# Performance work log

Hardware: AMD Instinct MI355X
Metric: run time of the kernel (lower is better)

The kernel has to match this reference:

```python
import jax, jax.numpy as jnp
import numpy as np

EPS = 1e-05
BITW = 8
BITA = 8


def _ste_round(v):
    # round with identity gradient (TF Round->Identity override)
    return v + jax.lax.stop_gradient(jnp.round(v) - v)


def _quantize_overflow(x, bits):
    # tensorlayer _quantize_overflow: linear quantization over [min, max]
    n = 2.0 ** bits - 1.0
    mx = jnp.max(x)
    mn = jnp.min(x)
    step = jax.lax.stop_gradient((mx - mn) / n)
    return _ste_round((x - mn) / step) * step + mn


def _conv2d_same(x, w):
    # x: [N,H,W,C], w: [KH,KW,C,F]
    return jax.lax.conv_general_dilated(
        x, w, window_strides=(1, 1), padding='SAME',
        dimension_numbers=('NHWC', 'HWIO', 'NHWC'))


def setup_inputs() -> dict:
    key = jax.random.key(0)
    k1, k2 = jax.random.split(key)
    x = jax.random.normal(k1, (32, 56, 56, 128), dtype=jnp.float32)
    W = jax.random.normal(k2, (3, 3, 128, 256), dtype=jnp.float32) * 0.02
    gamma = jnp.ones((256,), dtype=jnp.float32)
    beta = jnp.zeros((256,), dtype=jnp.float32)
    return {"x": x, "W": W, "gamma": gamma, "beta": beta}


def reference(x, W, gamma, beta):
    # 1) fake-quantize activations
    xq = _quantize_overflow(x, BITA)
    # 2) full-precision conv to get batch statistics (training path)
    conv_out = _conv2d_same(x, W)  # [N,H,W,F]
    mean = jnp.mean(conv_out, axis=(0, 1, 2))          # [F]
    var = jnp.var(conv_out, axis=(0, 1, 2))            # [F], biased (tf.nn.moments)
    inv_std = 1.0 / jnp.sqrt(var + EPS)                # [F]
    # 3) fold BN into weights/bias
    w_fold = W * (gamma * inv_std)                     # broadcast over [KH,KW,C,F]
    bias_fold = beta - gamma * mean * inv_std          # [F]
    # 4) quantize folded weights, conv with quantized activations
    wq = _quantize_overflow(w_fold, BITW)
    out = _conv2d_same(xq, wq) + bias_fold
    return jax.nn.relu(out)
```

## Files before the change

### kernel.cpp

```cpp
#include <hip/hip_runtime.h>

typedef float f32x4_t __attribute__((ext_vector_type(4)));
typedef __bf16 bf16x8_t __attribute__((ext_vector_type(8)));
typedef unsigned short u16x8_t __attribute__((ext_vector_type(8)));

#define NPIX        100352
#define PIX_PER_IMG 3136
#define PH          58
#define PPIX        3364
#define C_IN        128
#define C_OUT       256
#define NV4         3211264
#define NWELEM      294912
#define MTILES      392
#define NPADPIX     107648

#define OFF_ENC     0
#define OFF_SCALE   64
#define OFF_BIAS    1152
#define OFF_WT      4096
#define OFF_WQT     593920
#define OFF_PSUM    1183744
#define OFF_WFMIN   1585152
#define OFF_WFMAX   1586176
#define OFF_PSQ     1986560
#define OFF_XPAD    2789376
#define OFF_XQPAD   30347264

__device__ __forceinline__ unsigned short f2bf(float x) {
  unsigned u = __float_as_uint(x);
  u += 0x7FFFu + ((u >> 16) & 1u);
  return (unsigned short)(u >> 16);
}
__device__ __forceinline__ unsigned encf(float v) {
  unsigned u = __float_as_uint(v);
  return (u & 0x80000000u) ? ~u : (u | 0x80000000u);
}
__device__ __forceinline__ float decf(unsigned e) {
  unsigned u = (e & 0x80000000u) ? (e ^ 0x80000000u) : ~e;
  return __uint_as_float(u);
}
__device__ __forceinline__ void gl_lds16(const void* g, void* l) {
  auto gp = (const __attribute__((address_space(1))) unsigned*)(const unsigned*)g;
  auto lp = (__attribute__((address_space(3))) unsigned*)(unsigned*)l;
  __builtin_amdgcn_global_load_lds(gp, lp, 16, 0, 0);
}
#define SCHED_FENCE() __builtin_amdgcn_sched_barrier(0)

__global__ void kinit(unsigned* enc) {
  enc[0] = 0xFFFFFFFFu; enc[1] = 0u;
  enc[2] = 0xFFFFFFFFu; enc[3] = 0u;
}

__global__ void kminmax(const float4* __restrict__ x, unsigned* __restrict__ enc) {
  const int tid = blockIdx.x * blockDim.x + threadIdx.x;
  const int stride = gridDim.x * blockDim.x;
  float mn = 3.4e38f, mx = -3.4e38f;
  for (int i = tid; i < NV4; i += stride) {
    float4 v = x[i];
    mn = fminf(mn, fminf(fminf(v.x, v.y), fminf(v.z, v.w)));
    mx = fmaxf(mx, fmaxf(fmaxf(v.x, v.y), fmaxf(v.z, v.w)));
  }
  #pragma unroll
  for (int off = 32; off > 0; off >>= 1) {
    mn = fminf(mn, __shfl_xor(mn, off));
    mx = fmaxf(mx, __shfl_xor(mx, off));
  }
  __shared__ float smn[4], smx[4];
  const int lane = threadIdx.x & 63, w = threadIdx.x >> 6;
  if (lane == 0) { smn[w] = mn; smx[w] = mx; }
  __syncthreads();
  if (threadIdx.x == 0) {
    mn = fminf(fminf(smn[0], smn[1]), fminf(smn[2], smn[3]));
    mx = fmaxf(fmaxf(smx[0], smx[1]), fmaxf(smx[2], smx[3]));
    atomicMin(&enc[0], encf(mn));
    atomicMax(&enc[1], encf(mx));
  }
}

__global__ void kwq(const float* __restrict__ W, const float* __restrict__ scale,
                    const unsigned* __restrict__ enc, unsigned short* __restrict__ wqt) {
  const int idx = blockIdx.x * 256 + threadIdx.x;
  if (idx >= NWELEM) return;
  const int c = idx & 127;
  const int f = (idx >> 7) & 255;
  const int tap = idx >> 15;
  const float wmn = decf(enc[2]), wmx = decf(enc[3]);
  const float wstep = (wmx - wmn) / 255.0f;
  const float wrstep = 255.0f / (wmx - wmn);
  const float v = W[(tap * 128 + c) * 256 + f] * scale[f];
  const float q = rintf((v - wmn) * wrstep) * wstep + wmn;
  wqt[idx] = f2bf(q);
}

__global__ void kpadfill(const float* __restrict__ x, const unsigned* __restrict__ enc,
                         unsigned short* __restrict__ xpad, unsigned short* __restrict__ xqpad,
                         const float* __restrict__ W, unsigned short* __restrict__ wtt,
                         float* __restrict__ wfmin, float* __restrict__ wfmax)
{
  if (blockIdx.x >= 7880) {
    const int f = blockIdx.x - 7880;
    float mn = 3.4e38f, mx = -3.4e38f;
    for (int e = threadIdx.x; e < 1152; e += 256) {
      const float v = W[e * 256 + f];
      mn = fminf(mn, v); mx = fmaxf(mx, v);
    }
    #pragma unroll
    for (int off = 32; off > 0; off >>= 1) {
      mn = fminf(mn, __shfl_xor(mn, off));
      mx = fmaxf(mx, __shfl_xor(mx, off));
    }
    __shared__ float rmn[4], rmx[4];
    const int lane = threadIdx.x & 63, w = threadIdx.x >> 6;
    if (lane == 0) { rmn[w] = mn; rmx[w] = mx; }
    __syncthreads();
    if (threadIdx.x == 0) {
      wfmin[f] = fminf(fminf(rmn[0], rmn[1]), fminf(rmn[2], rmn[3]));
      wfmax[f] = fmaxf(fmaxf(rmx[0], rmx[1]), fmaxf(rmx[2], rmx[3]));
    }
    return;
  }
  if (blockIdx.x >= 6728) {
    const int idx = (blockIdx.x - 6728) * 256 + threadIdx.x;
    if (idx < NWELEM) {
      const int c = idx & 127;
      const int f = (idx >> 7) & 255;
      const int tap = idx >> 15;
      wtt[idx] = f2bf(W[(tap * 128 + c) * 256 + f]);
    }
    return;
  }
  const int tid = blockIdx.x * 256 + threadIdx.x;
  if (tid >= NPADPIX * 16) return;
  const int pp = tid >> 4;
  const int c8 = (tid & 15) << 3;
  const int n = pp / PPIX;
  const int rem = pp - n * PPIX;
  const int hp = rem / PH;
  const int wp = rem - hp * PH;
  u16x8_t vb, vq;
  #pragma unroll
  for (int j = 0; j < 8; ++j) { vb[j] = 0; vq[j] = 0; }
  if (hp >= 1 && hp <= 56 && wp >= 1 && wp <= 56) {
    const float mn = decf(enc[0]), mx = decf(enc[1]);
    const float step = (mx - mn) / 255.0f, rstep = 255.0f / (mx - mn);
    const float* src = x + ((n * PIX_PER_IMG) + (hp - 1) * 56 + (wp - 1)) * C_IN + c8;
    const float4 a = *(const float4*)src;
    const float4 b = *(const float4*)(src + 4);
    const float v[8] = {a.x, a.y, a.z, a.w, b.x, b.y, b.z, b.w};
    #pragma unroll
    for (int j = 0; j < 8; ++j) {
      vb[j] = f2bf(v[j]);
      const float qv = rintf((v[j] - mn) * rstep) * step + mn;
      vq[j] = f2bf(qv);
    }
  }
  *(u16x8_t*)(xpad + pp * C_IN + c8) = vb;
  *(u16x8_t*)(xqpad + pp * C_IN + c8) = vq;
}

template<int STATS>
__global__ __launch_bounds__(512, 4)
void kconv(const unsigned short* __restrict__ xin,
           const unsigned short* __restrict__ wt,
           float* __restrict__ out,
           const float* __restrict__ bias,
           float* __restrict__ psum,
           float* __restrict__ psq)
{
  const int bid = blockIdx.x;
  const int slot = (bid & 7) * 98 + (bid >> 3);
  const int bm = slot >> 1;
  const int bn = slot & 1;

  const int tid = threadIdx.x;
  const int lane = tid & 63;
  const int wid = tid >> 6;
  const int wm = wid >> 1;
  const int wn = wid & 1;
  const int l16 = lane & 15;
  const int rsub = lane >> 4;

  __shared__ __align__(16) unsigned char smem[49152];

  unsigned aoff[2];
  {
    const int arow0 = wid * 8 + (lane >> 3);
    const int pc = lane & 7;
    #pragma unroll
    for (int j = 0; j < 2; ++j) {
      const int row = j * 64 + arow0;
      const int lc = pc ^ (row & 7);
      const int pix = bm * 256 + row + 128 * (lc >> 2);
      const int n = pix / PIX_PER_IMG;
      const int rem = pix - n * PIX_PER_IMG;
      const int hh = rem / 56;
      const int ww = rem - hh * 56;
      aoff[j] = (unsigned)((n * PPIX + hh * PH + ww) * C_IN + (lc & 3) * 8);
    }
  }
  unsigned boff;
  {
    const int row = wid * 8 + (lane >> 3);
    const int pc = lane & 7;
    const int lc = pc ^ (row & 7);
    const int f = bn * 128 + row + 64 * (lc >> 2);
    boff = (unsigned)(f * C_IN + (lc & 3) * 8);
  }

  int a_rd[4], b_rd[4];
  #pragma unroll
  for (int im = 0; im < 4; ++im) {
    const int p = wm * 64 + im * 16 + l16;
    const int row = p & 127, half = p >> 7;
    const int phys = (half * 4 + rsub) ^ (row & 7);
    a_rd[im] = row * 128 + phys * 16;
  }
  #pragma unroll
  for (int in = 0; in < 4; ++in) {
    const int f = wn * 64 + in * 16 + l16;
    const int row = f & 63, half = f >> 6;
    const int phys = (half * 4 + rsub) ^ (row & 7);
    b_rd[in] = row * 128 + phys * 16;
  }

  f32x4_t acc[4][4];
  #pragma unroll
  for (int im = 0; im < 4; ++im)
    #pragma unroll
    for (int in = 0; in < 4; ++in)
      #pragma unroll
      for (int j = 0; j < 4; ++j) acc[im][in][j] = 0.f;

  auto stage = [&](int s) {
    const int tap = s >> 2;
    const int cq = (s & 3) * 32;
    const int kh = tap / 3, kw = tap - kh * 3;
    const unsigned atap = (unsigned)((kh * PH + kw) * C_IN + cq);
    const unsigned btap = (unsigned)(tap * (C_OUT * C_IN) + cq);
    unsigned char* sA = smem + (s & 1) * 24576;
    unsigned char* sB = sA + 16384;
    gl_lds16(xin + atap + aoff[0], sA + wid * 1024);
    gl_lds16(xin + atap + aoff[1], sA + 8192 + wid * 1024);
    gl_lds16(wt + btap + boff, sB + wid * 1024);
  };

  auto compute = [&](int s) {
    const unsigned char* sA = smem + (s & 1) * 24576;
    const unsigned char* sB = sA + 16384;
    bf16x8_t av[4], bv[4];
    #pragma unroll
    for (int im = 0; im < 4; ++im) av[im] = *(const bf16x8_t*)(sA + a_rd[im]);
    #pragma unroll
    for (int in = 0; in < 4; ++in) bv[in] = *(const bf16x8_t*)(sB + b_rd[in]);
    #pragma unroll
    for (int im = 0; im < 4; ++im)
      #pragma unroll
      for (int in = 0; in < 4; ++in)
        acc[im][in] = __builtin_amdgcn_mfma_f32_16x16x32_bf16(av[im], bv[in], acc[im][in], 0, 0, 0);
  };

  stage(0);
  stage(1);

  #pragma unroll 1
  for (int s = 0; s < 35; ++s) {
    asm volatile("s_waitcnt vmcnt(3)" ::: "memory");
    SCHED_FENCE();
    __builtin_amdgcn_s_barrier();
    SCHED_FENCE();
    compute(s);
    SCHED_FENCE();
    __builtin_amdgcn_s_barrier();
    SCHED_FENCE();
    if (s < 34) stage(s + 2);
  }
  asm volatile("s_waitcnt vmcnt(0)" ::: "memory");
  SCHED_FENCE();
  __builtin_amdgcn_s_barrier();
  SCHED_FENCE();
  compute(35);

  if (STATS) {
    __syncthreads();
    float* sb = (float*)smem;
    #pragma unroll
    for (int in = 0; in < 4; ++in) {
      float s = 0.f, q = 0.f;
      #pragma unroll
      for (int im = 0; im < 4; ++im)
        #pragma unroll
        for (int j = 0; j < 4; ++j) {
          const float v = acc[im][in][j];
          s += v; q += v * v;
        }
      s += __shfl_xor(s, 16); q += __shfl_xor(q, 16);
      s += __shfl_xor(s, 32); q += __shfl_xor(q, 32);
      if (lane < 16) {
        sb[wid * 64 + in * 16 + lane] = s;
        sb[512 + wid * 64 + in * 16 + lane] = q;
      }
    }
    __syncthreads();
    if (tid < 128) {
      const int wn2 = tid >> 6, cl = tid & 63;
      float s = 0.f, q = 0.f;
      #pragma unroll
      for (int wm2 = 0; wm2 < 4; ++wm2) {
        s += sb[(wm2 * 2 + wn2) * 64 + cl];
        q += sb[512 + (wm2 * 2 + wn2) * 64 + cl];
      }
      psum[(bm * 2 + bn) * 128 + tid] = s;
      psq[(bm * 2 + bn) * 128 + tid] = q;
    }
  } else {
    float bval[4];
    #pragma unroll
    for (int in = 0; in < 4; ++in)
      bval[in] = bias[bn * 128 + wn * 64 + in * 16 + l16];
    #pragma unroll
    for (int im = 0; im < 4; ++im) {
      #pragma unroll
      for (int j = 0; j < 4; ++j) {
        const int pix = bm * 256 + wm * 64 + im * 16 + rsub * 4 + j;
        #pragma unroll
        for (int in = 0; in < 4; ++in) {
          const int f = bn * 128 + wn * 64 + in * 16 + l16;
          out[pix * 256 + f] = fmaxf(acc[im][in][j] + bval[in], 0.f);
        }
      }
    }
  }
}

__global__ __launch_bounds__(256)
void kstats(const float* __restrict__ psum, const float* __restrict__ psq,
            const float* __restrict__ gamma, const float* __restrict__ beta,
            float* __restrict__ scale, float* __restrict__ bias,
            const float* __restrict__ wfmin, const float* __restrict__ wfmax,
            unsigned* __restrict__ enc)
{
  const int ch = blockIdx.x;
  const int bn = ch >> 7, col = ch & 127;
  float s = 0.f, q = 0.f;
  for (int bm = threadIdx.x; bm < MTILES; bm += 256) {
    s += psum[(bm * 2 + bn) * 128 + col];
    q += psq[(bm * 2 + bn) * 128 + col];
  }
  #pragma unroll
  for (int off = 32; off > 0; off >>= 1) {
    s += __shfl_xor(s, off);
    q += __shfl_xor(q, off);
  }
  __shared__ float ss[4], sq2[4];
  const int lane = threadIdx.x & 63, w = threadIdx.x >> 6;
  if (lane == 0) { ss[w] = s; sq2[w] = q; }
  __syncthreads();
  if (threadIdx.x == 0) {
    s = ss[0] + ss[1] + ss[2] + ss[3];
    q = sq2[0] + sq2[1] + sq2[2] + sq2[3];
    const float inv = 1.0f / (float)NPIX;
    const float mean = s * inv;
    const float var = q * inv - mean * mean;
    const float istd = 1.0f / sqrtf(var + 1e-5f);
    const float g = gamma[ch];
    const float sc = g * istd;
    scale[ch] = sc;
    bias[ch] = beta[ch] - g * mean * istd;
    const float p0 = sc * wfmin[ch];
    const float p1 = sc * wfmax[ch];
    atomicMin(&enc[2], encf(fminf(p0, p1)));
    atomicMax(&enc[3], encf(fmaxf(p0, p1)));
  }
}

extern "C" void kernel_launch(void* const* d_in, const int* in_sizes, int n_in,
                              void* d_out, int out_size, void* d_ws, size_t ws_size,
                              hipStream_t stream)
{
  const float* x     = (const float*)d_in[0];
  const float* W     = (const float*)d_in[1];
  const float* gamma = (const float*)d_in[2];
  const float* beta  = (const float*)d_in[3];
  float* out = (float*)d_out;
  char* ws = (char*)d_ws;

  unsigned* enc        = (unsigned*)(ws + OFF_ENC);
  float* scale         = (float*)(ws + OFF_SCALE);
  float* bias          = (float*)(ws + OFF_BIAS);
  unsigned short* Wt   = (unsigned short*)(ws + OFF_WT);
  unsigned short* Wqt  = (unsigned short*)(ws + OFF_WQT);
  float* psum          = (float*)(ws + OFF_PSUM);
  float* wfmin         = (float*)(ws + OFF_WFMIN);
  float* wfmax         = (float*)(ws + OFF_WFMAX);
  float* psq           = (float*)(ws + OFF_PSQ);
  unsigned short* xpad  = (unsigned short*)(ws + OFF_XPAD);
  unsigned short* xqpad = (unsigned short*)(ws + OFF_XQPAD);

  kinit<<<1, 64, 0, stream>>>(enc);
  kminmax<<<1024, 256, 0, stream>>>((const float4*)x, enc);
  kpadfill<<<8136, 256, 0, stream>>>(x, enc, xpad, xqpad, W, Wt, wfmin, wfmax);
  kconv<1><<<784, 512, 0, stream>>>(xpad, Wt, nullptr, nullptr, psum, psq);
  kstats<<<256, 256, 0, stream>>>(psum, psq, gamma, beta, scale, bias, wfmin, wfmax, enc);
  kwq<<<1152, 256, 0, stream>>>(W, scale, enc, Wqt);
  kconv<0><<<784, 512, 0, stream>>>(xqpad, Wqt, out, bias, nullptr, nullptr);
}
```

Before: 215.5 us.

## Shrink conv tiles to 128x128 and load weights directly into registers

The implicit-GEMM conv kernel moves from 512-thread 256x128 tiles to 256-thread 128x128 tiles, which doubles the grid to 1568 blocks and cuts LDS use to 16KB. The weight (B) operand no longer goes through shared memory. Each wave loads it straight from global memory into registers with inline global_load_dwordx4, double-buffered across two unrolled pipeline stages. This is meant to raise occupancy and drop LDS traffic for B, but each wave now fetches weights separately, so there is less reuse and more global and L2 load traffic. The partial-stats buffers and the stats reduction grow to match the doubled number of M tiles.

```diff
diff --git a/kernel.cpp b/kernel.cpp
--- a/kernel.cpp
+++ b/kernel.cpp
@@ -12,7 +12,7 @@
 #define C_OUT       256
 #define NV4         3211264
 #define NWELEM      294912
-#define MTILES      392
+#define MT128       784
 #define NPADPIX     107648
 
 #define OFF_ENC     0
@@ -21,11 +21,11 @@
 #define OFF_WT      4096
 #define OFF_WQT     593920
 #define OFF_PSUM    1183744
-#define OFF_WFMIN   1585152
-#define OFF_WFMAX   1586176
-#define OFF_PSQ     1986560
-#define OFF_XPAD    2789376
-#define OFF_XQPAD   30347264
+#define OFF_WFMIN   1988608
+#define OFF_WFMAX   1989632
+#define OFF_PSQ     1990656
+#define OFF_XPAD    2793472
+#define OFF_XQPAD   30351360
 
 __device__ __forceinline__ unsigned short f2bf(float x) {
   unsigned u = __float_as_uint(x);
@@ -160,7 +160,7 @@
 }
 
 template<int STATS>
-__global__ __launch_bounds__(512, 4)
+__global__ __launch_bounds__(256, 3)
 void kconv(const unsigned short* __restrict__ xin,
            const unsigned short* __restrict__ wt,
            float* __restrict__ out,
@@ -169,7 +169,7 @@
            float* __restrict__ psq)
 {
   const int bid = blockIdx.x;
-  const int slot = (bid & 7) * 98 + (bid >> 3);
+  const int slot = (bid & 7) * 196 + (bid >> 3);
   const int bm = slot >> 1;
   const int bn = slot & 1;
 
@@ -181,17 +181,16 @@
   const int l16 = lane & 15;
   const int rsub = lane >> 4;
 
-  __shared__ __align__(16) unsigned char smem[49152];
+  __shared__ __align__(16) unsigned char smem[16384];
 
   unsigned aoff[2];
   {
-    const int arow0 = wid * 8 + (lane >> 3);
-    const int pc = lane & 7;
+    const int pc = tid & 7;
     #pragma unroll
     for (int j = 0; j < 2; ++j) {
-      const int row = j * 64 + arow0;
+      const int row = j * 32 + (tid >> 3);
       const int lc = pc ^ (row & 7);
-      const int pix = bm * 256 + row + 128 * (lc >> 2);
+      const int pix = bm * 128 + row + 64 * (lc >> 2);
       const int n = pix / PIX_PER_IMG;
       const int rem = pix - n * PIX_PER_IMG;
       const int hh = rem / 56;
@@ -199,29 +198,19 @@
       aoff[j] = (unsigned)((n * PPIX + hh * PH + ww) * C_IN + (lc & 3) * 8);
     }
   }
-  unsigned boff;
-  {
-    const int row = wid * 8 + (lane >> 3);
-    const int pc = lane & 7;
-    const int lc = pc ^ (row & 7);
-    const int f = bn * 128 + row + 64 * (lc >> 2);
-    boff = (unsigned)(f * C_IN + (lc & 3) * 8);
-  }
-
-  int a_rd[4], b_rd[4];
+  int a_rd[4];
   #pragma unroll
   for (int im = 0; im < 4; ++im) {
     const int p = wm * 64 + im * 16 + l16;
-    const int row = p & 127, half = p >> 7;
+    const int row = p & 63, half = p >> 6;
     const int phys = (half * 4 + rsub) ^ (row & 7);
     a_rd[im] = row * 128 + phys * 16;
   }
+  unsigned boffB[4];
   #pragma unroll
   for (int in = 0; in < 4; ++in) {
-    const int f = wn * 64 + in * 16 + l16;
-    const int row = f & 63, half = f >> 6;
-    const int phys = (half * 4 + rsub) ^ (row & 7);
-    b_rd[in] = row * 128 + phys * 16;
+    const int f = bn * 128 + wn * 64 + in * 16 + l16;
+    boffB[in] = (unsigned)(f * C_IN + rsub * 8) * 2u;
   }
 
   f32x4_t acc[4][4];
@@ -237,22 +226,28 @@
     const int cq = (s & 3) * 32;
     const int kh = tap / 3, kw = tap - kh * 3;
     const unsigned atap = (unsigned)((kh * PH + kw) * C_IN + cq);
-    const unsigned btap = (unsigned)(tap * (C_OUT * C_IN) + cq);
-    unsigned char* sA = smem + (s & 1) * 24576;
-    unsigned char* sB = sA + 16384;
+    unsigned char* sA = smem + (s & 1) * 8192;
     gl_lds16(xin + atap + aoff[0], sA + wid * 1024);
-    gl_lds16(xin + atap + aoff[1], sA + 8192 + wid * 1024);
-    gl_lds16(wt + btap + boff, sB + wid * 1024);
+    gl_lds16(xin + atap + aoff[1], sA + 4096 + wid * 1024);
   };
 
-  auto compute = [&](int s) {
-    const unsigned char* sA = smem + (s & 1) * 24576;
-    const unsigned char* sB = sA + 16384;
-    bf16x8_t av[4], bv[4];
+  auto loadB = [&](int s, bf16x8_t (&bv)[4]) {
+    const int tap = s >> 2;
+    const int cq = (s & 3) * 32;
+    const unsigned short* base = wt + tap * (C_OUT * C_IN) + cq;
+    #pragma unroll
+    for (int in = 0; in < 4; ++in)
+      asm volatile("global_load_dwordx4 %0, %1, %2"
+                   : "=v"(bv[in])
+                   : "v"(boffB[in]), "s"(base)
+                   : "memory");
+  };
+
+  auto compute = [&](int s, bf16x8_t (&bv)[4]) {
+    const unsigned char* sA = smem + (s & 1) * 8192;
+    bf16x8_t av[4];
     #pragma unroll
     for (int im = 0; im < 4; ++im) av[im] = *(const bf16x8_t*)(sA + a_rd[im]);
-    #pragma unroll
-    for (int in = 0; in < 4; ++in) bv[in] = *(const bf16x8_t*)(sB + b_rd[in]);
     #pragma unroll
     for (int im = 0; im < 4; ++im)
       #pragma unroll
@@ -260,26 +255,32 @@
         acc[im][in] = __builtin_amdgcn_mfma_f32_16x16x32_bf16(av[im], bv[in], acc[im][in], 0, 0, 0);
   };
 
-  stage(0);
-  stage(1);
+  bf16x8_t bvA[4], bvB[4];
+  stage(0); loadB(0, bvA);
+  stage(1); loadB(1, bvB);
 
   #pragma unroll 1
-  for (int s = 0; s < 35; ++s) {
-    asm volatile("s_waitcnt vmcnt(3)" ::: "memory");
+  for (int s = 0; s < 36; s += 2) {
+    asm volatile("s_waitcnt vmcnt(6)" ::: "memory");
     SCHED_FENCE();
     __builtin_amdgcn_s_barrier();
     SCHED_FENCE();
-    compute(s);
+    compute(s, bvA);
     SCHED_FENCE();
     __builtin_amdgcn_s_barrier();
     SCHED_FENCE();
-    if (s < 34) stage(s + 2);
-  }
-  asm volatile("s_waitcnt vmcnt(0)" ::: "memory");
-  SCHED_FENCE();
-  __builtin_amdgcn_s_barrier();
-  SCHED_FENCE();
-  compute(35);
+    if (s + 2 < 36) { stage(s + 2); loadB(s + 2, bvA); }
+    if (s + 1 < 35) asm volatile("s_waitcnt vmcnt(6)" ::: "memory");
+    else            asm volatile("s_waitcnt vmcnt(0)" ::: "memory");
+    SCHED_FENCE();
+    __builtin_amdgcn_s_barrier();
+    SCHED_FENCE();
+    compute(s + 1, bvB);
+    SCHED_FENCE();
+    __builtin_amdgcn_s_barrier();
+    SCHED_FENCE();
+    if (s + 3 < 36) { stage(s + 3); loadB(s + 3, bvB); }
+  }
 
   if (STATS) {
     __syncthreads();
@@ -298,18 +299,14 @@
       s += __shfl_xor(s, 32); q += __shfl_xor(q, 32);
       if (lane < 16) {
         sb[wid * 64 + in * 16 + lane] = s;
-        sb[512 + wid * 64 + in * 16 + lane] = q;
+        sb[256 + wid * 64 + in * 16 + lane] = q;
       }
     }
     __syncthreads();
     if (tid < 128) {
       const int wn2 = tid >> 6, cl = tid & 63;
-      float s = 0.f, q = 0.f;
-      #pragma unroll
-      for (int wm2 = 0; wm2 < 4; ++wm2) {
-        s += sb[(wm2 * 2 + wn2) * 64 + cl];
-        q += sb[512 + (wm2 * 2 + wn2) * 64 + cl];
-      }
+      const float s = sb[wn2 * 64 + cl] + sb[(2 + wn2) * 64 + cl];
+      const float q = sb[256 + wn2 * 64 + cl] + sb[256 + (2 + wn2) * 64 + cl];
       psum[(bm * 2 + bn) * 128 + tid] = s;
       psq[(bm * 2 + bn) * 128 + tid] = q;
     }
@@ -322,7 +319,7 @@
     for (int im = 0; im < 4; ++im) {
       #pragma unroll
       for (int j = 0; j < 4; ++j) {
-        const int pix = bm * 256 + wm * 64 + im * 16 + rsub * 4 + j;
+        const int pix = bm * 128 + wm * 64 + im * 16 + rsub * 4 + j;
         #pragma unroll
         for (int in = 0; in < 4; ++in) {
           const int f = bn * 128 + wn * 64 + in * 16 + l16;
@@ -343,7 +340,7 @@
   const int ch = blockIdx.x;
   const int bn = ch >> 7, col = ch & 127;
   float s = 0.f, q = 0.f;
-  for (int bm = threadIdx.x; bm < MTILES; bm += 256) {
+  for (int bm = threadIdx.x; bm < MT128; bm += 256) {
     s += psum[(bm * 2 + bn) * 128 + col];
     q += psq[(bm * 2 + bn) * 128 + col];
   }
@@ -400,8 +397,8 @@
   kinit<<<1, 64, 0, stream>>>(enc);
   kminmax<<<1024, 256, 0, stream>>>((const float4*)x, enc);
   kpadfill<<<8136, 256, 0, stream>>>(x, enc, xpad, xqpad, W, Wt, wfmin, wfmax);
-  kconv<1><<<784, 512, 0, stream>>>(xpad, Wt, nullptr, nullptr, psum, psq);
+  kconv<1><<<1568, 256, 0, stream>>>(xpad, Wt, nullptr, nullptr, psum, psq);
   kstats<<<256, 256, 0, stream>>>(psum, psq, gamma, beta, scale, bias, wfmin, wfmax, enc);
   kwq<<<1152, 256, 0, stream>>>(W, scale, enc, Wqt);
-  kconv<0><<<784, 512, 0, stream>>>(xqpad, Wqt, out, bias, nullptr, nullptr);
-}
+  kconv<0><<<1568, 256, 0, stream>>>(xqpad, Wqt, out, bias, nullptr, nullptr);
+}
```

Result: slower. 333.6 us (+54.8%).

## Fuse min/max into padding pass and overlap quantized-input fill with stats conv

Applied to the files above, without the earlier changes.

Computes the activation min/max inside the bf16 padding kernel, so the separate min/max pass over x goes away. The quantized padded-input fill and the per-channel weight min/max move into extra blocks of the stats convolution launch, where they can overlap the GEMM blocks. The init kernel becomes a memset, and max is stored as min of the inverted encoding so that a single 0xFF fill initialises both slots. The cost is a larger, heterogeneous conv grid and a second read of x inside the conv launch.

```diff
diff --git a/kernel.cpp b/kernel.cpp
--- a/kernel.cpp
+++ b/kernel.cpp
@@ -10,7 +10,6 @@
 #define PPIX        3364
 #define C_IN        128
 #define C_OUT       256
-#define NV4         3211264
 #define NWELEM      294912
 #define MTILES      392
 #define NPADPIX     107648
@@ -47,20 +46,45 @@
 }
 #define SCHED_FENCE() __builtin_amdgcn_sched_barrier(0)
 
-__global__ void kinit(unsigned* enc) {
-  enc[0] = 0xFFFFFFFFu; enc[1] = 0u;
-  enc[2] = 0xFFFFFFFFu; enc[3] = 0u;
-}
-
-__global__ void kminmax(const float4* __restrict__ x, unsigned* __restrict__ enc) {
-  const int tid = blockIdx.x * blockDim.x + threadIdx.x;
-  const int stride = gridDim.x * blockDim.x;
+__global__ __launch_bounds__(256)
+void kprep1(const float* __restrict__ x, unsigned short* __restrict__ xpad,
+            const float* __restrict__ W, unsigned short* __restrict__ wtt,
+            unsigned* __restrict__ enc)
+{
+  if (blockIdx.x >= 6728) {
+    const int idx = (blockIdx.x - 6728) * 256 + threadIdx.x;
+    if (idx < NWELEM) {
+      const int c = idx & 127;
+      const int f = (idx >> 7) & 255;
+      const int tap = idx >> 15;
+      wtt[idx] = f2bf(W[(tap * 128 + c) * 256 + f]);
+    }
+    return;
+  }
+  const int tid = blockIdx.x * 256 + threadIdx.x;
+  const int pp = tid >> 4;
+  const int c8 = (tid & 15) << 3;
+  const int n = pp / PPIX;
+  const int rem = pp - n * PPIX;
+  const int hp = rem / PH;
+  const int wp = rem - hp * PH;
+  u16x8_t vb;
+  #pragma unroll
+  for (int j = 0; j < 8; ++j) vb[j] = 0;
   float mn = 3.4e38f, mx = -3.4e38f;
-  for (int i = tid; i < NV4; i += stride) {
-    float4 v = x[i];
-    mn = fminf(mn, fminf(fminf(v.x, v.y), fminf(v.z, v.w)));
-    mx = fmaxf(mx, fmaxf(fmaxf(v.x, v.y), fmaxf(v.z, v.w)));
-  }
+  if (hp >= 1 && hp <= 56 && wp >= 1 && wp <= 56) {
+    const float* src = x + ((n * PIX_PER_IMG) + (hp - 1) * 56 + (wp - 1)) * C_IN + c8;
+    const float4 a = *(const float4*)src;
+    const float4 b = *(const float4*)(src + 4);
+    const float v[8] = {a.x, a.y, a.z, a.w, b.x, b.y, b.z, b.w};
+    #pragma unroll
+    for (int j = 0; j < 8; ++j) {
+      vb[j] = f2bf(v[j]);
+      mn = fminf(mn, v[j]);
+      mx = fmaxf(mx, v[j]);
+    }
+  }
+  *(u16x8_t*)(xpad + pp * C_IN + c8) = vb;
   #pragma unroll
   for (int off = 32; off > 0; off >>= 1) {
     mn = fminf(mn, __shfl_xor(mn, off));
@@ -74,7 +98,7 @@
     mn = fminf(fminf(smn[0], smn[1]), fminf(smn[2], smn[3]));
     mx = fmaxf(fmaxf(smx[0], smx[1]), fmaxf(smx[2], smx[3]));
     atomicMin(&enc[0], encf(mn));
-    atomicMax(&enc[1], encf(mx));
+    atomicMin(&enc[1], ~encf(mx));
   }
 }
 
@@ -85,78 +109,12 @@
   const int c = idx & 127;
   const int f = (idx >> 7) & 255;
   const int tap = idx >> 15;
-  const float wmn = decf(enc[2]), wmx = decf(enc[3]);
+  const float wmn = decf(enc[2]), wmx = decf(~enc[3]);
   const float wstep = (wmx - wmn) / 255.0f;
   const float wrstep = 255.0f / (wmx - wmn);
   const float v = W[(tap * 128 + c) * 256 + f] * scale[f];
   const float q = rintf((v - wmn) * wrstep) * wstep + wmn;
   wqt[idx] = f2bf(q);
-}
-
-__global__ void kpadfill(const float* __restrict__ x, const unsigned* __restrict__ enc,
-                         unsigned short* __restrict__ xpad, unsigned short* __restrict__ xqpad,
-                         const float* __restrict__ W, unsigned short* __restrict__ wtt,
-                         float* __restrict__ wfmin, float* __restrict__ wfmax)
-{
-  if (blockIdx.x >= 7880) {
-    const int f = blockIdx.x - 7880;
-    float mn = 3.4e38f, mx = -3.4e38f;
-    for (int e = threadIdx.x; e < 1152; e += 256) {
-      const float v = W[e * 256 + f];
-      mn = fminf(mn, v); mx = fmaxf(mx, v);
-    }
-    #pragma unroll
-    for (int off = 32; off > 0; off >>= 1) {
-      mn = fminf(mn, __shfl_xor(mn, off));
-      mx = fmaxf(mx, __shfl_xor(mx, off));
-    }
-    __shared__ float rmn[4], rmx[4];
-    const int lane = threadIdx.x & 63, w = threadIdx.x >> 6;
-    if (lane == 0) { rmn[w] = mn; rmx[w] = mx; }
-    __syncthreads();
-    if (threadIdx.x == 0) {
-      wfmin[f] = fminf(fminf(rmn[0], rmn[1]), fminf(rmn[2], rmn[3]));
-      wfmax[f] = fmaxf(fmaxf(rmx[0], rmx[1]), fmaxf(rmx[2], rmx[3]));
-    }
-    return;
-  }
-  if (blockIdx.x >= 6728) {
-    const int idx = (blockIdx.x - 6728) * 256 + threadIdx.x;
-    if (idx < NWELEM) {
-      const int c = idx & 127;
-      const int f = (idx >> 7) & 255;
-      const int tap = idx >> 15;
-      wtt[idx] = f2bf(W[(tap * 128 + c) * 256 + f]);
-    }
-    return;
-  }
-  const int tid = blockIdx.x * 256 + threadIdx.x;
-  if (tid >= NPADPIX * 16) return;
-  const int pp = tid >> 4;
-  const int c8 = (tid & 15) << 3;
-  const int n = pp / PPIX;
-  const int rem = pp - n * PPIX;
-  const int hp = rem / PH;
-  const int wp = rem - hp * PH;
-  u16x8_t vb, vq;
-  #pragma unroll
-  for (int j = 0; j < 8; ++j) { vb[j] = 0; vq[j] = 0; }
-  if (hp >= 1 && hp <= 56 && wp >= 1 && wp <= 56) {
-    const float mn = decf(enc[0]), mx = decf(enc[1]);
-    const float step = (mx - mn) / 255.0f, rstep = 255.0f / (mx - mn);
-    const float* src = x + ((n * PIX_PER_IMG) + (hp - 1) * 56 + (wp - 1)) * C_IN + c8;
-    const float4 a = *(const float4*)src;
-    const float4 b = *(const float4*)(src + 4);
-    const float v[8] = {a.x, a.y, a.z, a.w, b.x, b.y, b.z, b.w};
-    #pragma unroll
-    for (int j = 0; j < 8; ++j) {
-      vb[j] = f2bf(v[j]);
-      const float qv = rintf((v[j] - mn) * rstep) * step + mn;
-      vq[j] = f2bf(qv);
-    }
-  }
-  *(u16x8_t*)(xpad + pp * C_IN + c8) = vb;
-  *(u16x8_t*)(xqpad + pp * C_IN + c8) = vq;
 }
 
 template<int STATS>
@@ -166,8 +124,69 @@
            float* __restrict__ out,
            const float* __restrict__ bias,
            float* __restrict__ psum,
-           float* __restrict__ psq)
+           float* __restrict__ psq,
+           const float* __restrict__ xsrc,
+           const unsigned* __restrict__ enc,
+           unsigned short* __restrict__ xqpad,
+           float* __restrict__ wfmin,
+           float* __restrict__ wfmax,
+           const float* __restrict__ Wsrc)
 {
+  __shared__ __align__(16) unsigned char smem[49152];
+
+  if (STATS && blockIdx.x >= 784) {
+    if (blockIdx.x < 784 + 3364) {
+      const int g = (blockIdx.x - 784) * 512 + threadIdx.x;
+      const int pp = g >> 4;
+      const int c8 = (g & 15) << 3;
+      const int n = pp / PPIX;
+      const int rem = pp - n * PPIX;
+      const int hp = rem / PH;
+      const int wp = rem - hp * PH;
+      u16x8_t vq;
+      #pragma unroll
+      for (int j = 0; j < 8; ++j) vq[j] = 0;
+      if (hp >= 1 && hp <= 56 && wp >= 1 && wp <= 56) {
+        const float mn = decf(enc[0]), mx = decf(~enc[1]);
+        const float step = (mx - mn) / 255.0f, rstep = 255.0f / (mx - mn);
+        const float* src = xsrc + ((n * PIX_PER_IMG) + (hp - 1) * 56 + (wp - 1)) * C_IN + c8;
+        const float4 a = *(const float4*)src;
+        const float4 b = *(const float4*)(src + 4);
+        const float v[8] = {a.x, a.y, a.z, a.w, b.x, b.y, b.z, b.w};
+        #pragma unroll
+        for (int j = 0; j < 8; ++j)
+          vq[j] = f2bf(rintf((v[j] - mn) * rstep) * step + mn);
+      }
+      *(u16x8_t*)(xqpad + pp * C_IN + c8) = vq;
+    } else {
+      const int f = blockIdx.x - (784 + 3364);
+      float mn = 3.4e38f, mx = -3.4e38f;
+      for (int e = (int)threadIdx.x; e < 1152; e += 512) {
+        const float v = Wsrc[e * 256 + f];
+        mn = fminf(mn, v); mx = fmaxf(mx, v);
+      }
+      #pragma unroll
+      for (int off = 32; off > 0; off >>= 1) {
+        mn = fminf(mn, __shfl_xor(mn, off));
+        mx = fmaxf(mx, __shfl_xor(mx, off));
+      }
+      float* sb = (float*)smem;
+      const int lane = threadIdx.x & 63, w = threadIdx.x >> 6;
+      if (lane == 0) { sb[w] = mn; sb[8 + w] = mx; }
+      __syncthreads();
+      if (threadIdx.x == 0) {
+        #pragma unroll
+        for (int i = 1; i < 8; ++i) {
+          mn = fminf(mn, sb[i]); mx = fmaxf(mx, sb[8 + i]);
+        }
+        mn = fminf(mn, sb[0]);
+        wfmin[f] = mn;
+        wfmax[f] = mx;
+      }
+    }
+    return;
+  }
+
   const int bid = blockIdx.x;
   const int slot = (bid & 7) * 98 + (bid >> 3);
   const int bm = slot >> 1;
@@ -180,8 +199,6 @@
   const int wn = wid & 1;
   const int l16 = lane & 15;
   const int rsub = lane >> 4;
-
-  __shared__ __align__(16) unsigned char smem[49152];
 
   unsigned aoff[2];
   {
@@ -370,7 +387,7 @@
     const float p0 = sc * wfmin[ch];
     const float p1 = sc * wfmax[ch];
     atomicMin(&enc[2], encf(fminf(p0, p1)));
-    atomicMax(&enc[3], encf(fmaxf(p0, p1)));
+    atomicMin(&enc[3], ~encf(fmaxf(p0, p1)));
   }
 }
 
@@ -397,11 +414,12 @@
   unsigned short* xpad  = (unsigned short*)(ws + OFF_XPAD);
   unsigned short* xqpad = (unsigned short*)(ws + OFF_XQPAD);
 
-  kinit<<<1, 64, 0, stream>>>(enc);
-  kminmax<<<1024, 256, 0, stream>>>((const float4*)x, enc);
-  kpadfill<<<8136, 256, 0, stream>>>(x, enc, xpad, xqpad, W, Wt, wfmin, wfmax);
-  kconv<1><<<784, 512, 0, stream>>>(xpad, Wt, nullptr, nullptr, psum, psq);
+  hipMemsetAsync(enc, 0xFF, 16, stream);
+  kprep1<<<7880, 256, 0, stream>>>(x, xpad, W, Wt, enc);
+  kconv<1><<<784 + 3364 + 256, 512, 0, stream>>>(xpad, Wt, nullptr, nullptr, psum, psq,
+                                                 x, enc, xqpad, wfmin, wfmax, W);
   kstats<<<256, 256, 0, stream>>>(psum, psq, gamma, beta, scale, bias, wfmin, wfmax, enc);
   kwq<<<1152, 256, 0, stream>>>(W, scale, enc, Wqt);
-  kconv<0><<<784, 512, 0, stream>>>(xqpad, Wqt, out, bias, nullptr, nullptr);
-}
+  kconv<0><<<784, 512, 0, stream>>>(xqpad, Wqt, out, bias, nullptr, nullptr,
+                                    nullptr, nullptr, nullptr, nullptr, nullptr, nullptr);
+}
```

Measured after the change: 319.4 us. +48.2%, slower.
